# Kernel tuning notes

Hardware: AMD Instinct MI355X
Metric: run time of the kernel (lower is better)

The kernel has to match this reference:

```python
import jax, jax.numpy as jnp
import numpy as np

NUM_HEADS = 32
NUM_KV_HEADS = 8
HEAD_DIM = 128
ROPE_BASE = 10000.0


def rotate_half(x):
    half = x.shape[-1] // 2
    x1, x2 = x[..., :half], x[..., half:]
    return jnp.concatenate((-x2, x1), axis=-1)


def rope_cos_sin(position_ids, head_dim, dtype):
    # inv_freq: [head_dim/2]
    inv_freq = 1.0 / (ROPE_BASE ** (jnp.arange(0, head_dim, 2, dtype=jnp.float32) / head_dim))
    freqs = position_ids.astype(jnp.float32)[..., None] * inv_freq  # [B, S, hd/2]
    emb = jnp.concatenate((freqs, freqs), axis=-1)                  # [B, S, hd]
    # add head axis -> [B, 1, S, hd]
    return jnp.cos(emb)[:, None].astype(dtype), jnp.sin(emb)[:, None].astype(dtype)


def setup_inputs() -> dict:
    key = jax.random.key(0)
    k_x, k_q, k_k, k_v, k_o = jax.random.split(key, 5)
    B, S, H = 1, 2048, 4096
    w_scale = 0.02
    return {
        "hidden_states": jax.random.normal(k_x, (B, S, H), dtype=jnp.float32),
        "position_ids": jnp.broadcast_to(jnp.arange(S, dtype=jnp.int32), (B, S)),
        "Wq": jax.random.normal(k_q, (NUM_HEADS * HEAD_DIM, H), dtype=jnp.float32) * w_scale,
        "Wk": jax.random.normal(k_k, (NUM_KV_HEADS * HEAD_DIM, H), dtype=jnp.float32) * w_scale,
        "Wv": jax.random.normal(k_v, (NUM_KV_HEADS * HEAD_DIM, H), dtype=jnp.float32) * w_scale,
        "Wo": jax.random.normal(k_o, (H, NUM_HEADS * HEAD_DIM), dtype=jnp.float32) * w_scale,
    }


def reference(hidden_states, position_ids, Wq, Wk, Wv, Wo):
    B, S, H = hidden_states.shape
    n_rep = NUM_HEADS // NUM_KV_HEADS

    # projections (torch Linear: y = x @ W.T), reshape to [B, heads, S, hd]
    q = (hidden_states @ Wq.T).reshape(B, S, NUM_HEADS, HEAD_DIM).transpose(0, 2, 1, 3)
    k = (hidden_states @ Wk.T).reshape(B, S, NUM_KV_HEADS, HEAD_DIM).transpose(0, 2, 1, 3)
    v = (hidden_states @ Wv.T).reshape(B, S, NUM_KV_HEADS, HEAD_DIM).transpose(0, 2, 1, 3)

    cos, sin = rope_cos_sin(position_ids, HEAD_DIM, hidden_states.dtype)
    q = q * cos + rotate_half(q) * sin
    k = k * cos + rotate_half(k) * sin

    # repeat_kv: GQA expansion to [B, NUM_HEADS, S, hd]
    k = jnp.repeat(k, n_rep, axis=1)
    v = jnp.repeat(v, n_rep, axis=1)

    scale = 1.0 / jnp.sqrt(jnp.asarray(HEAD_DIM, dtype=hidden_states.dtype))
    scores = jnp.einsum('bhqd,bhkd->bhqk', q, k) * scale  # [B, H, S, S]

    # causal additive mask
    causal = jnp.tril(jnp.ones((S, S), dtype=bool))
    scores = jnp.where(causal[None, None], scores, jnp.finfo(scores.dtype).min)

    probs = jax.nn.softmax(scores, axis=-1)
    attn = jnp.einsum('bhqk,bhkd->bhqd', probs, v)         # [B, H, S, hd]
    attn = attn.transpose(0, 2, 1, 3).reshape(B, S, NUM_HEADS * HEAD_DIM)
    return attn @ Wo.T
```

## Files before the change

kernel.cpp:

```cpp
#include <hip/hip_runtime.h>
#include <hip/hip_bf16.h>
#include <stdint.h>

typedef __bf16 bf16;
typedef __attribute__((ext_vector_type(8))) __bf16 bf16x8;
typedef __attribute__((ext_vector_type(4))) __bf16 bf16x4;
typedef __attribute__((ext_vector_type(4))) float f32x4;
typedef __attribute__((ext_vector_type(16))) float f32x16;
typedef __attribute__((ext_vector_type(4))) unsigned int uint4v;

#define S_LEN 2048
#define HDIM  4096
#define NQH   32
#define NKVH  8
#define DHEAD 128
#define QKVN  6144
#define KOFF  4096
#define VOFF  5120
#define NSPLIT 4

__device__ __forceinline__ void gload_lds16(const bf16* g, bf16* l) {
  __builtin_amdgcn_global_load_lds(
      (const __attribute__((address_space(1))) unsigned int*)g,
      (__attribute__((address_space(3))) unsigned int*)l, 16, 0, 0);
}

__global__ __launch_bounds__(256) void cvt_f32_bf16(const float* __restrict__ in,
                                                    bf16* __restrict__ out, int n4) {
  int i = blockIdx.x * 256 + threadIdx.x;
  if (i >= n4) return;
  float4 v = ((const float4*)in)[i];
  bf16x4 ov = {(bf16)v.x, (bf16)v.y, (bf16)v.z, (bf16)v.w};
  *(bf16x4*)&out[(size_t)i * 4] = ov;
}

__global__ __launch_bounds__(256) void rope_table(const int* __restrict__ pos,
                                                  float* __restrict__ tab) {
  int idx = blockIdx.x * 256 + threadIdx.x;
  int i = idx & 63, s = idx >> 6;
  float p = (float)pos[s];
  float invf = powf(10000.0f, -(float)i * (1.0f / 64.0f));
  float ang = p * invf;
  tab[idx * 2]     = cosf(ang);
  tab[idx * 2 + 1] = sinf(ang);
}

__global__ __launch_bounds__(256) void rope_apply(bf16* __restrict__ QKV,
                                                  const float* __restrict__ tab) {
  int idx = blockIdx.x * 256 + threadIdx.x;
  int dp = idx & 63;
  int t = idx >> 6;
  int head = t % 40;
  int s = t / 40;
  float c  = tab[(s * 64 + dp) * 2];
  float sn = tab[(s * 64 + dp) * 2 + 1];
  size_t base = (size_t)s * QKVN + head * DHEAD;
  float x0 = (float)QKV[base + dp];
  float x1 = (float)QKV[base + 64 + dp];
  QKV[base + dp]      = (bf16)(x0 * c - x1 * sn);
  QKV[base + 64 + dp] = (bf16)(x1 * c + x0 * sn);
}

__global__ __launch_bounds__(256) void transpose_v(const bf16* __restrict__ QKV,
                                                   bf16* __restrict__ Vt) {
  __shared__ bf16 t[64][72];
  int tid = threadIdx.x;
  int bs = blockIdx.x * 64, bc = blockIdx.y * 64;
  int sl = tid >> 3, cb = (tid & 7) * 8;
#pragma unroll
  for (int ss = 0; ss < 64; ss += 32) {
    int s = sl + ss;
    *(bf16x8*)&t[s][cb] = *(const bf16x8*)&QKV[(size_t)(bs + s) * QKVN + VOFF + bc + cb];
  }
  __syncthreads();
  int cl = tid >> 3, sb = (tid & 7) * 8;
#pragma unroll
  for (int cc = 0; cc < 64; cc += 32) {
    int c = cl + cc;
    bf16x8 v;
#pragma unroll
    for (int k = 0; k < 8; ++k) v[k] = t[sb + k][c];
    *(bf16x8*)&Vt[(size_t)(bc + c) * S_LEN + bs + sb] = v;
  }
}

template <typename OutT, int BN>
__global__ __launch_bounds__(512, 2) void gemm_ph(const bf16* __restrict__ A,
                                                  const bf16* __restrict__ B,
                                                  OutT* __restrict__ C,
                                                  int M, int N, int K) {
  constexpr int NJ = BN / 64;
  constexpr int NJH = NJ / 2;
  constexpr int LB = BN / 64;
  constexpr int WCW = BN / 4;
  __shared__ bf16 Al[3][128 * 64];
  __shared__ bf16 Bl[2][BN * 64];
  const int tid = threadIdx.x;
  const int w = tid >> 6, lane = tid & 63;
  const int r = lane & 15, g = lane >> 4;
  const int wr = w >> 2, wc = w & 3;
  const int id = blockIdx.x;
  const int xcd = id & 7, o = id >> 3;
  const int by = o >> 1, bx = xcd * 2 + (o & 1);
  const int bm = by * 128, bn = bx * BN;

  f32x4 acc[4][NJ];
#pragma unroll
  for (int mi = 0; mi < 4; ++mi)
#pragma unroll
    for (int nj = 0; nj < NJ; ++nj) acc[mi][nj] = (f32x4){0.f, 0.f, 0.f, 0.f};

  auto stageA = [&](int slot, int k0) {
#pragma unroll
    for (int j = 0; j < 2; ++j) {
      int chunk = (j * 8 + w) * 64 + lane;
      int row = chunk >> 3, c = chunk & 7;
      gload_lds16(&A[(size_t)(bm + row) * K + k0 + ((c ^ (row & 7)) << 3)],
                  &Al[slot][(j * 8 + w) * 512]);
    }
  };
  auto stageB = [&](int buf, int k0, int i0, int i1) {
#pragma unroll
    for (int i = 0; i < LB; ++i) {
      if (i < i0 || i >= i1) continue;
      int chunk = (i * 8 + w) * 64 + lane;
      int row = chunk >> 3, c = chunk & 7;
      gload_lds16(&B[(size_t)(bn + row) * K + k0 + ((c ^ (row & 7)) << 3)],
                  &Bl[buf][(i * 8 + w) * 512]);
    }
  };

  const int NT = K >> 6;
  stageA(0, 0);
  stageB(0, 0, 0, LB);
  stageA(1, 64);
  asm volatile("s_waitcnt vmcnt(2)" ::: "memory");
  __builtin_amdgcn_s_barrier();
  asm volatile("" ::: "memory");

  for (int t = 0; t < NT; ++t) {
    const bf16* Ac = Al[t % 3];
    const bf16* Bc = Bl[t & 1];
    const bool p1 = (t + 1 < NT), p2 = (t + 2 < NT);
    const int kn = (t + 1) << 6;
    bf16x8 af[4], bfr[NJH];

#pragma unroll
    for (int p = 0; p < 4; ++p) {
      const int ks = p >> 1, njh = p & 1;
      if (njh == 0) {
#pragma unroll
        for (int mi = 0; mi < 4; ++mi) {
          int row = wr * 64 + mi * 16 + r;
          af[mi] = *(const bf16x8*)&Ac[row * 64 + (((ks * 4 + g) ^ (row & 7)) << 3)];
        }
      }
#pragma unroll
      for (int nj = 0; nj < NJH; ++nj) {
        int row = wc * WCW + (njh * NJH + nj) * 16 + r;
        bfr[nj] = *(const bf16x8*)&Bc[row * 64 + (((ks * 4 + g) ^ (row & 7)) << 3)];
      }
      if (p == 0 && p1) stageB((t + 1) & 1, kn, 0, 2);
      if (p == 1 && p1) stageB((t + 1) & 1, kn, 2, 4);
      if (p == 2 && p1) stageB((t + 1) & 1, kn, 4, LB);
      if (p == 3 && p2) stageA((t + 2) % 3, (t + 2) << 6);
      __builtin_amdgcn_s_barrier();
      asm volatile("s_waitcnt lgkmcnt(0)" ::: "memory");
      __builtin_amdgcn_s_setprio(1);
#pragma unroll
      for (int mi = 0; mi < 4; ++mi)
#pragma unroll
        for (int nj = 0; nj < NJH; ++nj)
          acc[mi][njh * NJH + nj] = __builtin_amdgcn_mfma_f32_16x16x32_bf16(
              af[mi], bfr[nj], acc[mi][njh * NJH + nj], 0, 0, 0);
      __builtin_amdgcn_s_setprio(0);
      __builtin_amdgcn_s_barrier();
      asm volatile("" ::: "memory");
    }
    if (p2) asm volatile("s_waitcnt vmcnt(2)" ::: "memory");
    else    asm volatile("s_waitcnt vmcnt(0)" ::: "memory");
    __builtin_amdgcn_s_barrier();
    asm volatile("" ::: "memory");
  }

#pragma unroll
  for (int mi = 0; mi < 4; ++mi)
#pragma unroll
    for (int nj = 0; nj < NJ; ++nj)
#pragma unroll
      for (int j = 0; j < 4; ++j) {
        int row = bm + wr * 64 + mi * 16 + g * 4 + j;
        int col = bn + wc * WCW + nj * 16 + r;
        C[(size_t)row * N + col] = (OutT)acc[mi][nj][j];
      }
}

__global__ __launch_bounds__(256) void attn_kernel(const bf16* __restrict__ QKV,
                                                   const bf16* __restrict__ Vt,
                                                   bf16* __restrict__ Opart,
                                                   float* __restrict__ Mpart,
                                                   float* __restrict__ Lpart) {
  __shared__ bf16 Kl[3][32 * 128];
  __shared__ bf16 Vl[3][128 * 32];
  const int tid = threadIdx.x;
  const int w = tid >> 6, lane = tid & 63;
  const int l31 = lane & 31, hi = lane >> 5;
  const int bx = blockIdx.x;
  const int kvh = bx & 7;
  const int rest = bx >> 3;
  const int s = rest & 3;
  const int qblk = 63 - (rest >> 2);
  const int h = kvh * 4 + w;
  const int q0 = qblk * 32;
  const int pid = (h * 64 + qblk) * NSPLIT + s;
  const float scale = 0.12751746f;

  const int nt = qblk + 1;
  const int t0 = (nt * s) >> 2;
  const int t1 = (nt * (s + 1)) >> 2;

  f32x16 o[4];
#pragma unroll
  for (int t = 0; t < 4; ++t)
#pragma unroll
    for (int r = 0; r < 16; ++r) o[t][r] = 0.f;
  float m_run = -1e30f, l_run = 0.f;

  auto stage = [&](int bufi, int kv0) {
#pragma unroll
    for (int ii = 0; ii < 2; ++ii) {
      int ins = w * 2 + ii;
      int hr = ins * 8 + (lane >> 3);
      int kvrow = hr >> 1, hK = hr & 1;
      int gk = ((lane & 7) ^ (kvrow & 7)) + 8 * hK;
      gload_lds16(&QKV[(size_t)(kv0 + kvrow) * QKVN + KOFF + kvh * DHEAD + gk * 8],
                  &Kl[bufi][ins * 512]);
      int pr = ins * 8 + (lane >> 3);
      int xv = (lane & 7) ^ (pr & 7);
      int dV = pr * 2 + (xv >> 2);
      gload_lds16(&Vt[(size_t)(kvh * DHEAD + dV) * S_LEN + kv0 + (xv & 3) * 8],
                  &Vl[bufi][ins * 512]);
    }
  };

  if (t0 < t1) {
    bf16x8 qf[8];
#pragma unroll
    for (int k8 = 0; k8 < 8; ++k8) {
      bf16x8 raw = *(const bf16x8*)&QKV[(size_t)(q0 + l31) * QKVN + h * DHEAD + k8 * 16 + hi * 8];
#pragma unroll
      for (int e = 0; e < 8; ++e) qf[k8][e] = (bf16)((float)raw[e] * scale);
    }

    int cur = t0 % 3;
    stage(cur, t0 * 32);
    if (t0 + 1 < t1) {
      stage(cur == 2 ? 0 : cur + 1, (t0 + 1) * 32);
      asm volatile("s_waitcnt vmcnt(4)" ::: "memory");
    } else {
      asm volatile("s_waitcnt vmcnt(0)" ::: "memory");
    }
    __builtin_amdgcn_s_barrier();
    asm volatile("" ::: "memory");

    for (int t = t0; t < t1; ++t) {
      if (t + 2 < t1) {
        int s2 = cur ? cur - 1 : 2;
        stage(s2, (t + 2) * 32);
      }

      f32x16 st;
#pragma unroll
      for (int r = 0; r < 16; ++r) st[r] = 0.f;
      __builtin_amdgcn_s_setprio(1);
#pragma unroll
      for (int k8 = 0; k8 < 8; ++k8) {
        int g = 2 * k8 + hi;
        bf16x8 kf = *(const bf16x8*)&Kl[cur][l31 * 128 + (g >> 3) * 64 +
                                             (((g & 7) ^ (l31 & 7)) << 3)];
        st = __builtin_amdgcn_mfma_f32_32x32x16_bf16(kf, qf[k8], st, 0, 0, 0);
      }
      __builtin_amdgcn_s_setprio(0);

      if (t == nt - 1) {
#pragma unroll
        for (int r = 0; r < 16; ++r) {
          int kvr = (r & 3) + 8 * (r >> 2) + 4 * hi;
          if (kvr > l31) st[r] = -1e30f;
        }
      }
      float pmax = st[0];
#pragma unroll
      for (int r = 1; r < 16; ++r) pmax = fmaxf(pmax, st[r]);
      pmax = fmaxf(pmax, __shfl_xor(pmax, 32));
      if (!__all(pmax - m_run <= 8.0f)) {
        float mnew = fmaxf(m_run, pmax);
        float corr = exp2f(m_run - mnew);
        m_run = mnew;
        l_run *= corr;
#pragma unroll
        for (int r = 0; r < 16; ++r) {
          float cr = __shfl(corr, (r & 3) + 8 * (r >> 2) + 4 * hi);
          o[0][r] *= cr; o[1][r] *= cr; o[2][r] *= cr; o[3][r] *= cr;
        }
      }
      float rs = 0.f;
#pragma unroll
      for (int r = 0; r < 16; ++r) { st[r] = exp2f(st[r] - m_run); rs += st[r]; }
      rs += __shfl_xor(rs, 32);
      l_run += rs;
      bf16x8 pf0, pf1;
      {
        unsigned int A0[4], X0[4];
#pragma unroll
        for (int j = 0; j < 4; ++j) {
          unsigned short lo = __builtin_bit_cast(unsigned short, (bf16)st[2 * j]);
          unsigned short hi16 = __builtin_bit_cast(unsigned short, (bf16)st[2 * j + 1]);
          A0[j] = (unsigned int)lo | ((unsigned int)hi16 << 16);
        }
#pragma unroll
        for (int j = 0; j < 4; ++j) X0[j] = __shfl_xor(A0[j], 32);
        uint4v w0v = {hi ? X0[2] : A0[0], hi ? X0[3] : A0[1],
                      hi ? A0[2] : X0[0], hi ? A0[3] : X0[1]};
        pf0 = __builtin_bit_cast(bf16x8, w0v);
      }
      {
        unsigned int A1[4], X1[4];
#pragma unroll
        for (int j = 0; j < 4; ++j) {
          unsigned short lo = __builtin_bit_cast(unsigned short, (bf16)st[8 + 2 * j]);
          unsigned short hi16 = __builtin_bit_cast(unsigned short, (bf16)st[9 + 2 * j]);
          A1[j] = (unsigned int)lo | ((unsigned int)hi16 << 16);
        }
#pragma unroll
        for (int j = 0; j < 4; ++j) X1[j] = __shfl_xor(A1[j], 32);
        uint4v w1v = {hi ? X1[2] : A1[0], hi ? X1[3] : A1[1],
                      hi ? A1[2] : X1[0], hi ? A1[3] : X1[1]};
        pf1 = __builtin_bit_cast(bf16x8, w1v);
      }
      __builtin_amdgcn_s_setprio(1);
#pragma unroll
      for (int tt = 0; tt < 4; ++tt) {
        int pr = tt * 16 + (l31 >> 1);
        int sb4 = (l31 & 1) << 2;
        bf16x8 v0 = *(const bf16x8*)&Vl[cur][pr * 64 + (((sb4 + hi) ^ (pr & 7)) << 3)];
        bf16x8 v1 = *(const bf16x8*)&Vl[cur][pr * 64 + (((sb4 + 2 + hi) ^ (pr & 7)) << 3)];
        o[tt] = __builtin_amdgcn_mfma_f32_32x32x16_bf16(pf0, v0, o[tt], 0, 0, 0);
        o[tt] = __builtin_amdgcn_mfma_f32_32x32x16_bf16(pf1, v1, o[tt], 0, 0, 0);
      }
      __builtin_amdgcn_s_setprio(0);

      if (t + 2 < t1) {
        asm volatile("s_waitcnt vmcnt(4)" ::: "memory");
      } else {
        asm volatile("s_waitcnt vmcnt(0)" ::: "memory");
      }
      __builtin_amdgcn_s_barrier();
      asm volatile("" ::: "memory");
      cur = (cur == 2) ? 0 : cur + 1;
    }
  }

  float linv = (l_run > 0.f) ? 1.0f / l_run : 0.f;
  if (hi == 0) {
    Mpart[pid * 32 + l31] = m_run;
    Lpart[pid * 32 + l31] = l_run;
  }
#pragma unroll
  for (int r = 0; r < 16; ++r) {
    int qloc = (r & 3) + 8 * (r >> 2) + 4 * hi;
    float li = __shfl(linv, qloc);
    size_t row = (size_t)pid * (32 * DHEAD) + (size_t)qloc * DHEAD;
#pragma unroll
    for (int t2 = 0; t2 < 4; ++t2)
      Opart[row + t2 * 32 + l31] = (bf16)(o[t2][r] * li);
  }
}

__global__ __launch_bounds__(256) void attn_merge(const bf16* __restrict__ Opart,
                                                  const float* __restrict__ Mpart,
                                                  const float* __restrict__ Lpart,
                                                  bf16* __restrict__ Oout) {
  const int bx = blockIdx.x;
  const int h = bx >> 6, qblk = bx & 63;
  const int tid = threadIdx.x;
  const int r = tid >> 3, cseg = (tid & 7) * 16;
  const int pid0 = bx * NSPLIT;
  float m[NSPLIT], l[NSPLIT];
  float M = -1e30f;
#pragma unroll
  for (int s = 0; s < NSPLIT; ++s) {
    m[s] = Mpart[(pid0 + s) * 32 + r];
    l[s] = Lpart[(pid0 + s) * 32 + r];
    M = fmaxf(M, m[s]);
  }
  float wsum = 0.f, wv[NSPLIT];
#pragma unroll
  for (int s = 0; s < NSPLIT; ++s) { wv[s] = l[s] * exp2f(m[s] - M); wsum += wv[s]; }
  float inv = 1.0f / wsum;
#pragma unroll
  for (int s = 0; s < NSPLIT; ++s) wv[s] *= inv;
  size_t dst = (size_t)(qblk * 32 + r) * HDIM + h * DHEAD + cseg;
#pragma unroll
  for (int half = 0; half < 2; ++half) {
    float acc[8];
#pragma unroll
    for (int e = 0; e < 8; ++e) acc[e] = 0.f;
#pragma unroll
    for (int s = 0; s < NSPLIT; ++s) {
      bf16x8 a = *(const bf16x8*)&Opart[(size_t)(pid0 + s) * (32 * DHEAD) +
                                        (size_t)r * DHEAD + cseg + half * 8];
#pragma unroll
      for (int e = 0; e < 8; ++e) acc[e] += wv[s] * (float)a[e];
    }
    bf16x8 out;
#pragma unroll
    for (int e = 0; e < 8; ++e) out[e] = (bf16)acc[e];
    *(bf16x8*)&Oout[dst + half * 8] = out;
  }
}

extern "C" void kernel_launch(void* const* d_in, const int* in_sizes, int n_in,
                              void* d_out, int out_size, void* d_ws, size_t ws_size,
                              hipStream_t stream) {
  const float* X   = (const float*)d_in[0];
  const int*   pos = (const int*)d_in[1];
  const float* Wq  = (const float*)d_in[2];
  const float* Wk  = (const float*)d_in[3];
  const float* Wv  = (const float*)d_in[4];
  const float* Wo  = (const float*)d_in[5];
  float* out = (float*)d_out;
  char* ws = (char*)d_ws;

  size_t off = 0;
  bf16* Xb    = (bf16*)(ws + off); off += (size_t)2048 * 4096 * 2;
  bf16* Wqkvb = (bf16*)(ws + off); off += (size_t)6144 * 4096 * 2;
  bf16* Wob   = (bf16*)(ws + off); off += (size_t)4096 * 4096 * 2;
  bf16* QKV   = (bf16*)(ws + off); off += (size_t)2048 * 6144 * 2;
  bf16* Vt    = (bf16*)(ws + off); off += (size_t)1024 * 2048 * 2;
  bf16* attnb = (bf16*)(ws + off); off += (size_t)2048 * 4096 * 2;
  float* tab  = (float*)(ws + off); off += (size_t)2048 * 64 * 2 * 4;
  float* Mpart = (float*)(ws + off); off += (size_t)8192 * 32 * 4;
  float* Lpart = (float*)(ws + off); off += (size_t)8192 * 32 * 4;

  bf16* Opart = (bf16*)Xb;

  cvt_f32_bf16<<<2048 * 4096 / 4 / 256, 256, 0, stream>>>(X, Xb, 2048 * 4096 / 4);
  cvt_f32_bf16<<<4096 * 4096 / 4 / 256, 256, 0, stream>>>(Wq, Wqkvb, 4096 * 4096 / 4);
  cvt_f32_bf16<<<1024 * 4096 / 4 / 256, 256, 0, stream>>>(Wk, Wqkvb + (size_t)4096 * 4096,
                                                          1024 * 4096 / 4);
  cvt_f32_bf16<<<1024 * 4096 / 4 / 256, 256, 0, stream>>>(Wv, Wqkvb + (size_t)5120 * 4096,
                                                          1024 * 4096 / 4);
  cvt_f32_bf16<<<4096 * 4096 / 4 / 256, 256, 0, stream>>>(Wo, Wob, 4096 * 4096 / 4);
  rope_table<<<2048 * 64 / 256, 256, 0, stream>>>(pos, tab);
  gemm_ph<bf16, 384><<<256, 512, 0, stream>>>(Xb, Wqkvb, QKV, 2048, QKVN, 4096);
  rope_apply<<<2048 * 40 * 64 / 256, 256, 0, stream>>>(QKV, tab);
  transpose_v<<<dim3(2048 / 64, 1024 / 64), 256, 0, stream>>>(QKV, Vt);
  attn_kernel<<<2048, 256, 0, stream>>>(QKV, Vt, Opart, Mpart, Lpart);
  attn_merge<<<2048, 256, 0, stream>>>(Opart, Mpart, Lpart, attnb);
  gemm_ph<float, 256><<<256, 512, 0, stream>>>(attnb, Wob, out, 2048, 4096, 4096);
}
```

Before: 371.5 us.

## Fuse conversions, apply Q RoPE inside attention, swap QKV GEMM kernel

Merges the five fp32-to-bf16 conversion launches into one kernel. Moves the RoPE rotation for Q into the attention kernel's Q load, so the standalone RoPE pass only touches the K heads. Replaces the pipelined 128x384 QKV GEMM with a simpler single-buffered 128x128 GEMM using XCD-striped block mapping. That GEMM drops the multi-stage LDS pipelining and so may lose latency hiding, while the fusions cut launches and one read-write pass over Q.

```diff
diff --git a/kernel.cpp b/kernel.cpp
--- a/kernel.cpp
+++ b/kernel.cpp
@@ -25,13 +25,24 @@
       (__attribute__((address_space(3))) unsigned int*)l, 16, 0, 0);
 }
 
-__global__ __launch_bounds__(256) void cvt_f32_bf16(const float* __restrict__ in,
-                                                    bf16* __restrict__ out, int n4) {
-  int i = blockIdx.x * 256 + threadIdx.x;
-  if (i >= n4) return;
-  float4 v = ((const float4*)in)[i];
+__global__ __launch_bounds__(256) void cvt_all(const float* __restrict__ X,
+                                               const float* __restrict__ Wq,
+                                               const float* __restrict__ Wk,
+                                               const float* __restrict__ Wv,
+                                               const float* __restrict__ Wo,
+                                               bf16* __restrict__ Xb,
+                                               bf16* __restrict__ Wqkvb,
+                                               bf16* __restrict__ Wob) {
+  size_t i = (size_t)blockIdx.x * 256 + threadIdx.x;
+  const float* src; bf16* dst;
+  if (i < 2097152)       { src = X;  dst = Xb; }
+  else if (i < 6291456)  { i -= 2097152; src = Wq; dst = Wqkvb; }
+  else if (i < 7340032)  { i -= 6291456; src = Wk; dst = Wqkvb + (size_t)4096 * 4096; }
+  else if (i < 8388608)  { i -= 7340032; src = Wv; dst = Wqkvb + (size_t)5120 * 4096; }
+  else                   { i -= 8388608; src = Wo; dst = Wob; }
+  float4 v = ((const float4*)src)[i];
   bf16x4 ov = {(bf16)v.x, (bf16)v.y, (bf16)v.z, (bf16)v.w};
-  *(bf16x4*)&out[(size_t)i * 4] = ov;
+  *(bf16x4*)&dst[i * 4] = ov;
 }
 
 __global__ __launch_bounds__(256) void rope_table(const int* __restrict__ pos,
@@ -45,16 +56,16 @@
   tab[idx * 2 + 1] = sinf(ang);
 }
 
-__global__ __launch_bounds__(256) void rope_apply(bf16* __restrict__ QKV,
-                                                  const float* __restrict__ tab) {
+__global__ __launch_bounds__(256) void rope_k(bf16* __restrict__ QKV,
+                                              const float* __restrict__ tab) {
   int idx = blockIdx.x * 256 + threadIdx.x;
   int dp = idx & 63;
   int t = idx >> 6;
-  int head = t % 40;
-  int s = t / 40;
+  int kvh = t & 7;
+  int s = t >> 3;
   float c  = tab[(s * 64 + dp) * 2];
   float sn = tab[(s * 64 + dp) * 2 + 1];
-  size_t base = (size_t)s * QKVN + head * DHEAD;
+  size_t base = (size_t)s * QKVN + KOFF + kvh * DHEAD;
   float x0 = (float)QKV[base + dp];
   float x1 = (float)QKV[base + 64 + dp];
   QKV[base + dp]      = (bf16)(x0 * c - x1 * sn);
@@ -82,6 +93,75 @@
     for (int k = 0; k < 8; ++k) v[k] = t[sb + k][c];
     *(bf16x8*)&Vt[(size_t)(bc + c) * S_LEN + bs + sb] = v;
   }
+}
+
+template <typename OutT>
+__global__ __launch_bounds__(256) void gemm_bt(const bf16* __restrict__ A,
+                                               const bf16* __restrict__ B,
+                                               OutT* __restrict__ C,
+                                               int M, int N, int K, int NX) {
+  __shared__ bf16 At[128 * 64];
+  __shared__ bf16 Bt[128 * 64];
+  const int tid = threadIdx.x;
+  const int w = tid >> 6, lane = tid & 63;
+  const int r = lane & 15, g = lane >> 4;
+  const int id = blockIdx.x;
+  const int xcd = id & 7, o = id >> 3;
+  const int stripe = NX >> 3;
+  const int bxi = xcd * stripe + o % stripe;
+  const int byi = o / stripe;
+  const int bm = byi * 128, bn = bxi * 128;
+  const int wm = (w >> 1) * 64, wn = (w & 1) * 64;
+  f32x4 acc[4][4];
+#pragma unroll
+  for (int i = 0; i < 4; ++i)
+#pragma unroll
+    for (int j = 0; j < 4; ++j) acc[i][j] = (f32x4){0.f, 0.f, 0.f, 0.f};
+
+  const int chunk0 = w * 256 + lane;
+
+  for (int k0 = 0; k0 < K; k0 += 64) {
+#pragma unroll
+    for (int i = 0; i < 4; ++i) {
+      int chunk = chunk0 + i * 64;
+      int row = chunk >> 3, c8 = chunk & 7;
+      int cs = ((c8 ^ (row & 7)) << 3) + k0;
+      gload_lds16(&A[(size_t)(bm + row) * K + cs], &At[(w * 4 + i) * 512]);
+      gload_lds16(&B[(size_t)(bn + row) * K + cs], &Bt[(w * 4 + i) * 512]);
+    }
+    __syncthreads();
+#pragma unroll
+    for (int ks = 0; ks < 2; ++ks) {
+      bf16x8 af[4], bfr[4];
+#pragma unroll
+      for (int mi = 0; mi < 4; ++mi) {
+        int row = wm + mi * 16 + r;
+        af[mi] = *(const bf16x8*)&At[row * 64 + ((((ks << 2) + g) ^ (row & 7)) << 3)];
+      }
+#pragma unroll
+      for (int nj = 0; nj < 4; ++nj) {
+        int row = wn + nj * 16 + r;
+        bfr[nj] = *(const bf16x8*)&Bt[row * 64 + ((((ks << 2) + g) ^ (row & 7)) << 3)];
+      }
+#pragma unroll
+      for (int mi = 0; mi < 4; ++mi)
+#pragma unroll
+        for (int nj = 0; nj < 4; ++nj)
+          acc[mi][nj] = __builtin_amdgcn_mfma_f32_16x16x32_bf16(af[mi], bfr[nj],
+                                                                acc[mi][nj], 0, 0, 0);
+    }
+    __syncthreads();
+  }
+#pragma unroll
+  for (int mi = 0; mi < 4; ++mi)
+#pragma unroll
+    for (int nj = 0; nj < 4; ++nj)
+#pragma unroll
+      for (int j = 0; j < 4; ++j) {
+        int row = bm + wm + mi * 16 + g * 4 + j;
+        int col = bn + wn + nj * 16 + r;
+        C[(size_t)row * N + col] = (OutT)acc[mi][nj][j];
+      }
 }
 
 template <typename OutT, int BN>
@@ -197,6 +277,7 @@
 
 __global__ __launch_bounds__(256) void attn_kernel(const bf16* __restrict__ QKV,
                                                    const bf16* __restrict__ Vt,
+                                                   const float* __restrict__ tab,
                                                    bf16* __restrict__ Opart,
                                                    float* __restrict__ Mpart,
                                                    float* __restrict__ Lpart) {
@@ -245,11 +326,28 @@
 
   if (t0 < t1) {
     bf16x8 qf[8];
-#pragma unroll
-    for (int k8 = 0; k8 < 8; ++k8) {
-      bf16x8 raw = *(const bf16x8*)&QKV[(size_t)(q0 + l31) * QKVN + h * DHEAD + k8 * 16 + hi * 8];
-#pragma unroll
-      for (int e = 0; e < 8; ++e) qf[k8][e] = (bf16)((float)raw[e] * scale);
+    {
+      bf16x8 raw[8];
+#pragma unroll
+      for (int k8 = 0; k8 < 8; ++k8)
+        raw[k8] = *(const bf16x8*)&QKV[(size_t)(q0 + l31) * QKVN + h * DHEAD +
+                                       k8 * 16 + hi * 8];
+#pragma unroll
+      for (int k8 = 0; k8 < 4; ++k8) {
+        const float* tb = &tab[((size_t)(q0 + l31) * 64 + k8 * 16 + hi * 8) * 2];
+        float4 t0v = ((const float4*)tb)[0];
+        float4 t1v = ((const float4*)tb)[1];
+        float4 t2v = ((const float4*)tb)[2];
+        float4 t3v = ((const float4*)tb)[3];
+        float cs[8] = {t0v.x, t0v.z, t1v.x, t1v.z, t2v.x, t2v.z, t3v.x, t3v.z};
+        float sn[8] = {t0v.y, t0v.w, t1v.y, t1v.w, t2v.y, t2v.w, t3v.y, t3v.w};
+#pragma unroll
+        for (int e = 0; e < 8; ++e) {
+          float lo = (float)raw[k8][e], up = (float)raw[k8 + 4][e];
+          qf[k8][e]     = (bf16)((lo * cs[e] - up * sn[e]) * scale);
+          qf[k8 + 4][e] = (bf16)((up * cs[e] + lo * sn[e]) * scale);
+        }
+      }
     }
 
     int cur = t0 % 3;
@@ -445,18 +543,12 @@
 
   bf16* Opart = (bf16*)Xb;
 
-  cvt_f32_bf16<<<2048 * 4096 / 4 / 256, 256, 0, stream>>>(X, Xb, 2048 * 4096 / 4);
-  cvt_f32_bf16<<<4096 * 4096 / 4 / 256, 256, 0, stream>>>(Wq, Wqkvb, 4096 * 4096 / 4);
-  cvt_f32_bf16<<<1024 * 4096 / 4 / 256, 256, 0, stream>>>(Wk, Wqkvb + (size_t)4096 * 4096,
-                                                          1024 * 4096 / 4);
-  cvt_f32_bf16<<<1024 * 4096 / 4 / 256, 256, 0, stream>>>(Wv, Wqkvb + (size_t)5120 * 4096,
-                                                          1024 * 4096 / 4);
-  cvt_f32_bf16<<<4096 * 4096 / 4 / 256, 256, 0, stream>>>(Wo, Wob, 4096 * 4096 / 4);
+  cvt_all<<<49152, 256, 0, stream>>>(X, Wq, Wk, Wv, Wo, Xb, Wqkvb, Wob);
   rope_table<<<2048 * 64 / 256, 256, 0, stream>>>(pos, tab);
-  gemm_ph<bf16, 384><<<256, 512, 0, stream>>>(Xb, Wqkvb, QKV, 2048, QKVN, 4096);
-  rope_apply<<<2048 * 40 * 64 / 256, 256, 0, stream>>>(QKV, tab);
+  gemm_bt<bf16><<<768, 256, 0, stream>>>(Xb, Wqkvb, QKV, 2048, QKVN, 4096, 48);
+  rope_k<<<2048 * 8 * 64 / 256, 256, 0, stream>>>(QKV, tab);
   transpose_v<<<dim3(2048 / 64, 1024 / 64), 256, 0, stream>>>(QKV, Vt);
-  attn_kernel<<<2048, 256, 0, stream>>>(QKV, Vt, Opart, Mpart, Lpart);
+  attn_kernel<<<2048, 256, 0, stream>>>(QKV, Vt, tab, Opart, Mpart, Lpart);
   attn_merge<<<2048, 256, 0, stream>>>(Opart, Mpart, Lpart, attnb);
   gemm_ph<float, 256><<<256, 512, 0, stream>>>(attnb, Wob, out, 2048, 4096, 4096);
 }
```

New measurement: 378.4 us. About the same (+1.8%).
